# Kernel tuning notes

Measured on AMD Instinct MI355X. Metric: run time of the kernel, lower is better.

The kernel has to match this reference:

```python
import jax, jax.numpy as jnp
import numpy as np

NUM_GROUPS = 256


def _linear(x, w, b):
    return x @ w + b


def _layernorm(x, g, b, eps=1e-5):
    mu = jnp.mean(x, axis=-1, keepdims=True)
    var = jnp.mean((x - mu) ** 2, axis=-1, keepdims=True)
    return (x - mu) / jnp.sqrt(var + eps) * g + b


def setup_inputs() -> dict:
    key = jax.random.key(0)
    ks = jax.random.split(key, 12)
    B, N, C = 16, 8192, 3
    s = 0.02
    return {
        "xyz": jax.random.normal(ks[0], (B, N, C), jnp.float32),
        "labels": jax.random.randint(ks[1], (B, N), 0, NUM_GROUPS),
        # conv1: Linear(3,128) -> LayerNorm(128) -> ReLU -> Linear(128,256)
        "w1a": jax.random.normal(ks[2], (3, 128), jnp.float32) * s,
        "b1a": jnp.zeros((128,), jnp.float32),
        "g1": jnp.ones((128,), jnp.float32),
        "beta1": jnp.zeros((128,), jnp.float32),
        "w1b": jax.random.normal(ks[3], (128, 256), jnp.float32) * s,
        "b1b": jnp.zeros((256,), jnp.float32),
        # conv2: Linear(512,512) -> LayerNorm(512) -> ReLU -> Linear(512,256)
        "w2a": jax.random.normal(ks[4], (512, 512), jnp.float32) * s,
        "b2a": jnp.zeros((512,), jnp.float32),
        "g2": jnp.ones((512,), jnp.float32),
        "beta2": jnp.zeros((512,), jnp.float32),
        "w2b": jax.random.normal(ks[5], (512, 256), jnp.float32) * s,
        "b2b": jnp.zeros((256,), jnp.float32),
    }


def reference(xyz, labels, w1a, b1a, g1, beta1, w1b, b1b,
              w2a, b2a, g2, beta2, w2b, b2b):
    # per-batch segment reductions over cluster labels
    seg_sum = jax.vmap(lambda f, l: jax.ops.segment_sum(f, l, num_segments=NUM_GROUPS))
    seg_max = jax.vmap(lambda f, l: jax.ops.segment_max(f, l, num_segments=NUM_GROUPS))
    gather = jax.vmap(lambda p, l: p[l])  # [G,D],[N] -> [N,D]

    # centroids = per-cluster mean of xyz (converged kmeans centroids)
    counts = seg_sum(jnp.ones_like(xyz[..., :1]), labels)          # [B,G,1]
    centroids = seg_sum(xyz, labels) / jnp.maximum(counts, 1.0)    # [B,G,3]

    p_i = gather(centroids, labels)                                # [B,N,3]
    relative_xyz = xyz - p_i                                       # feature_type='dp'

    h = _linear(relative_xyz, w1a, b1a)
    h = jax.nn.relu(_layernorm(h, g1, beta1))
    h = _linear(h, w1b, b1b)                                       # [B,N,256]

    pooled = seg_max(h, labels)                                    # [B,G,256]
    pooled = jnp.where(jnp.isfinite(pooled), pooled, 0.0)          # empty groups -> 0
    repeated = gather(pooled, labels)                              # [B,N,256]

    cat = jnp.concatenate([repeated, h], axis=-1)                  # [B,N,512]
    h2 = _linear(cat, w2a, b2a)
    h2 = jax.nn.relu(_layernorm(h2, g2, beta2))
    h2 = _linear(h2, w2b, b2b)                                     # [B,N,256]

    out = seg_max(h2, labels)                                      # [B,G,256]
    out = jnp.where(jnp.isfinite(out), out, 0.0)
    return (centroids, out, p_i, labels)
```

## Files before the change

kernel.cpp:

```cpp
#include <hip/hip_runtime.h>
#include <hip/hip_bf16.h>

#define NB_  16
#define NPTS 8192
#define NG   256
#define NP   (NB_*NPTS)
#define NBLK (NP/32)

#define OFF_CENT 0
#define OFF_OUT  12288
#define OFF_PI   1060864
#define OFF_LAB  1454080

typedef unsigned short u16;
typedef __attribute__((ext_vector_type(8))) short bf16x8;
typedef __attribute__((ext_vector_type(4))) float f32x4;

static constexpr size_t WS_SUMS  = 0;
static constexpr size_t WS_A1    = 65536;
static constexpr size_t WS_H     = WS_A1   + (size_t)NP*128*2;
static constexpr size_t WS_PBF   = WS_H    + (size_t)NP*256*2;
static constexpr size_t WS_WT1   = WS_PBF  + (size_t)NB_*NG*256*2;
static constexpr size_t WS_WT2A  = WS_WT1  + (size_t)256*128*2;
static constexpr size_t WS_WT2B  = WS_WT2A + (size_t)512*512*2;
static constexpr size_t WS_PREP  = WS_WT2B + (size_t)256*512*2;
static constexpr size_t WS_OFFS  = WS_PREP + (size_t)NB_*NG*512*4;
static constexpr size_t WS_CNT   = WS_OFFS + (size_t)NB_*NG*4;
static constexpr size_t WS_CUR   = WS_CNT  + (size_t)NB_*NG*4;
static constexpr size_t WS_SPOS  = WS_CUR  + (size_t)NB_*NG*4;
static constexpr size_t WS_GLAB  = WS_SPOS + (size_t)NP*4;
static constexpr size_t WS_PF    = WS_GLAB + (size_t)NP*4;
static constexpr size_t WS_PL    = WS_PF   + (size_t)NBLK*256*4;
static constexpr size_t WS_DST   = WS_PL   + (size_t)NBLK*256*4;
static constexpr size_t WS_NEED  = WS_DST  + (size_t)NB_*NG*256*4;

__device__ __forceinline__ u16 f2bf_bits(float f){
  __hip_bfloat16 h = __float2bfloat16(f);
  union { __hip_bfloat16 h; u16 s; } u; u.h = h; return u.s;
}
__device__ __forceinline__ float bf_bits2f(u16 s){
  return __uint_as_float(((unsigned)s) << 16);
}

__device__ __forceinline__ void gload16(const void* g, void* l){
  __builtin_amdgcn_global_load_lds((const __attribute__((address_space(1))) void*)g,
                                   (__attribute__((address_space(3))) void*)l, 16, 0, 0);
}

__global__ void k_init(float* __restrict__ sums, int* __restrict__ cursor){
  int i = blockIdx.x*blockDim.x + threadIdx.x;
  if (i < NB_*NG*4) sums[i] = 0.f;
  if (i < NB_*NG) cursor[i] = 0;
}

__global__ void k_wt(const float* __restrict__ src, u16* __restrict__ dst, int K, int N){
  int i = blockIdx.x*blockDim.x + threadIdx.x;
  if (i >= K*N) return;
  int n = i / K, k = i - n*K;
  dst[i] = f2bf_bits(src[(size_t)k*N + n]);
}

__global__ void k_points(const float* __restrict__ xyz, const int* __restrict__ labels,
                         float* __restrict__ sums, float* __restrict__ outLab){
  int p = blockIdx.x*blockDim.x + threadIdx.x;
  if (p >= NP) return;
  int b = p / NPTS;
  int g = labels[p];
  float x = xyz[p*3+0], y = xyz[p*3+1], z = xyz[p*3+2];
  float* s = sums + (size_t)(b*NG + g)*4;
  atomicAdd(s+0, x); atomicAdd(s+1, y); atomicAdd(s+2, z); atomicAdd(s+3, 1.f);
  outLab[p] = (float)g;
}

__global__ void k_cent(const float* __restrict__ sums, float* __restrict__ cent_out){
  int i = blockIdx.x*blockDim.x + threadIdx.x;
  if (i >= NB_*NG) return;
  const float* s = sums + (size_t)i*4;
  float c = fmaxf(s[3], 1.f);
  cent_out[i*3+0] = s[0]/c;
  cent_out[i*3+1] = s[1]/c;
  cent_out[i*3+2] = s[2]/c;
}

__global__ void k_scan(const float* __restrict__ sums, int* __restrict__ offs,
                       int* __restrict__ counts){
  __shared__ int sc[256];
  int b = blockIdx.x, g = threadIdx.x;
  int c = (int)(sums[(size_t)(b*NG+g)*4+3] + 0.5f);
  sc[g] = c;
  __syncthreads();
  for (int d = 1; d < 256; d <<= 1){
    int t = (g >= d) ? sc[g-d] : 0;
    __syncthreads();
    sc[g] += t;
    __syncthreads();
  }
  offs[b*NG+g] = b*NPTS + sc[g] - c;
  counts[b*NG+g] = c;
}

__global__ void k_scatter(const int* __restrict__ labels, const int* __restrict__ offs,
                          int* __restrict__ cursor, int* __restrict__ sortpos,
                          int* __restrict__ glab){
  int p = blockIdx.x*blockDim.x + threadIdx.x;
  if (p >= NP) return;
  int b = p / NPTS, g = labels[p];
  int pos = offs[b*NG+g] + atomicAdd(&cursor[b*NG+g], 1);
  sortpos[p] = pos;
  glab[pos] = g;
}

__global__ __launch_bounds__(256) void k_mlp1(
    const float* __restrict__ xyz, const int* __restrict__ labels,
    const int* __restrict__ sortpos, const float* __restrict__ cent,
    const float* __restrict__ w1a, const float* __restrict__ b1a,
    const float* __restrict__ g1, const float* __restrict__ beta1,
    u16* __restrict__ a1, float* __restrict__ pi_out)
{
  int wave = (int)((blockIdx.x*blockDim.x + threadIdx.x) >> 6);
  int lane = threadIdx.x & 63;
  int p = wave;
  if (p >= NP) return;
  int b = p / NPTS;
  int g = labels[p];
  const float* cb = cent + (size_t)(b*NG+g)*3;
  float c0 = cb[0], c1 = cb[1], c2 = cb[2];
  float r0 = xyz[p*3+0]-c0, r1 = xyz[p*3+1]-c1, r2 = xyz[p*3+2]-c2;
  if (lane < 3) pi_out[(size_t)p*3+lane] = (lane==0?c0:(lane==1?c1:c2));
  int j = lane*2;
  float2 wa0 = *(const float2*)(w1a + 0*128 + j);
  float2 wa1 = *(const float2*)(w1a + 1*128 + j);
  float2 wa2 = *(const float2*)(w1a + 2*128 + j);
  float2 bb  = *(const float2*)(b1a + j);
  float t0 = bb.x + r0*wa0.x + r1*wa1.x + r2*wa2.x;
  float t1 = bb.y + r0*wa0.y + r1*wa1.y + r2*wa2.y;
  float s = t0+t1, sq = t0*t0 + t1*t1;
  #pragma unroll
  for (int m = 32; m; m >>= 1){ s += __shfl_xor(s, m); sq += __shfl_xor(sq, m); }
  float mu  = s * (1.f/128.f);
  float var = sq * (1.f/128.f) - mu*mu;
  float inv = rsqrtf(var + 1e-5f);
  float2 gg = *(const float2*)(g1 + j), be = *(const float2*)(beta1 + j);
  float a0 = fmaxf((t0-mu)*inv*gg.x + be.x, 0.f);
  float a1v = fmaxf((t1-mu)*inv*gg.y + be.y, 0.f);
  unsigned pk = ((unsigned)f2bf_bits(a1v) << 16) | f2bf_bits(a0);
  int sp = sortpos[p];
  *reinterpret_cast<unsigned*>(a1 + (size_t)sp*128 + j) = pk;
}

template<int EPI>
__global__ __launch_bounds__(256)
void mgemm(const u16* __restrict__ A, int lda, int K,
           const u16* __restrict__ BT, int ldb, int kofs,
           const float* __restrict__ bias,
           u16* __restrict__ Cst, float* __restrict__ Cf, int ldc, int Nc)
{
  __shared__ alignas(16) u16 As[128*32];
  __shared__ alignas(16) u16 Bs[128*32];
  int NBk = Nc >> 7;
  int bm = blockIdx.x / NBk, bn = blockIdx.x % NBk;
  int m0 = bm << 7, n0 = bn << 7;
  int tid = threadIdx.x;
  int lane = tid & 63, w = tid >> 6;
  int wr = w >> 1, wc = w & 1;
  int l15 = lane & 15, l4 = lane >> 4;
  int r0 = tid >> 2;
  int ks = (tid & 3) << 3;
  u16* asd0 = As + (size_t)(w*64)*8;
  u16* asd1 = As + (size_t)(256 + w*64)*8;
  u16* bsd0 = Bs + (size_t)(w*64)*8;
  u16* bsd1 = Bs + (size_t)(256 + w*64)*8;
  f32x4 acc[4][4];
  #pragma unroll
  for (int i = 0; i < 4; ++i)
    #pragma unroll
    for (int jj = 0; jj < 4; ++jj)
      #pragma unroll
      for (int e = 0; e < 4; ++e) acc[i][jj][e] = 0.f;

  for (int k0 = 0; k0 < K; k0 += 32){
    gload16(A + (size_t)(m0 + r0)*lda + k0 + ks, asd0);
    gload16(A + (size_t)(m0 + r0 + 64)*lda + k0 + ks, asd1);
    gload16(BT + (size_t)(n0 + r0)*ldb + kofs + k0 + ks, bsd0);
    gload16(BT + (size_t)(n0 + r0 + 64)*ldb + kofs + k0 + ks, bsd1);
    __syncthreads();
    bf16x8 af[4], bfr[4];
    #pragma unroll
    for (int i = 0; i < 4; ++i){
      af[i]  = *(const bf16x8*)&As[(size_t)(wr*64 + i*16 + l15)*32 + l4*8];
      bfr[i] = *(const bf16x8*)&Bs[(size_t)(wc*64 + i*16 + l15)*32 + l4*8];
    }
    #pragma unroll
    for (int i = 0; i < 4; ++i)
      #pragma unroll
      for (int jj = 0; jj < 4; ++jj)
        acc[i][jj] = __builtin_amdgcn_mfma_f32_16x16x32_bf16(af[i], bfr[jj], acc[i][jj], 0, 0, 0);
    __syncthreads();
  }

  float bi[4];
  #pragma unroll
  for (int jj = 0; jj < 4; ++jj) bi[jj] = bias[n0 + wc*64 + jj*16 + l15];
  #pragma unroll
  for (int i = 0; i < 4; ++i){
    #pragma unroll
    for (int r = 0; r < 4; ++r){
      int m = m0 + wr*64 + i*16 + l4*4 + r;
      #pragma unroll
      for (int jj = 0; jj < 4; ++jj){
        int n = n0 + wc*64 + jj*16 + l15;
        float v = acc[i][jj][r] + bi[jj];
        if (EPI == 1) Cst[(size_t)m*ldc + n] = f2bf_bits(v);
        if (EPI == 3) Cf[(size_t)m*ldc + n] = v;
      }
    }
  }
}

__global__ __launch_bounds__(256) void k_pool(const u16* __restrict__ h,
                                              const int* __restrict__ offs,
                                              const int* __restrict__ counts,
                                              u16* __restrict__ poolbf){
  int bg = blockIdx.x, c = threadIdx.x;
  int cnt = counts[bg];
  if (cnt == 0){ poolbf[(size_t)bg*256 + c] = 0; return; }
  int off = offs[bg];
  float mx = bf_bits2f(h[(size_t)off*256 + c]);
  for (int r = 1; r < cnt; ++r)
    mx = fmaxf(mx, bf_bits2f(h[(size_t)(off+r)*256 + c]));
  poolbf[(size_t)bg*256 + c] = f2bf_bits(mx);
}

__global__ __launch_bounds__(512, 4)
void fused3(const u16* __restrict__ h, const u16* __restrict__ wt2a,
            const u16* __restrict__ wt2b, const float* __restrict__ prepf,
            const float* __restrict__ b2b, const float* __restrict__ g2,
            const float* __restrict__ beta2, const int* __restrict__ glab,
            float* __restrict__ pf, float* __restrict__ pl, float* __restrict__ dstage)
{
  __shared__ alignas(16) char smem[33792];
  float* ssum  = (float*)(smem + 33280);
  float* ssq   = (float*)(smem + 33408);
  int*  glab_s = (int*)(smem + 33536);
  int tid = threadIdx.x;
  int w = tid >> 6, lane = tid & 63;
  int l15 = lane & 15, l4 = lane >> 4;
  int m0 = blockIdx.x << 5;
  if (tid < 32){ ssum[tid] = 0.f; ssq[tid] = 0.f; glab_s[tid] = glab[m0 + tid]; }

  const char* hb = (const char*)h;
  {
    int lrow = lane >> 5;
    int kb = (lane & 31) << 4;
    #pragma unroll
    for (int t = 0; t < 2; ++t){
      int q = w*2 + t;
      int row = q*2 + lrow;
      gload16(hb + (size_t)(m0 + row)*512 + (kb ^ ((row & 7) << 4)),
              smem + q*1024);
    }
  }
  f32x4 acc[2][4];
  #pragma unroll
  for (int i = 0; i < 2; ++i)
    #pragma unroll
    for (int j = 0; j < 4; ++j)
      #pragma unroll
      for (int e = 0; e < 4; ++e) acc[i][j][e] = 0.f;
  __syncthreads();

  for (int k0 = 0; k0 < 256; k0 += 32){
    bf16x8 af[2], bfr[4];
    #pragma unroll
    for (int i = 0; i < 2; ++i){
      int row = i*16 + l15;
      af[i] = *(const bf16x8*)(smem + row*512 + (((k0 + l4*8) << 1) ^ ((row & 7) << 4)));
    }
    #pragma unroll
    for (int j = 0; j < 4; ++j){
      int n = (w<<6) + (j<<4) + l15;
      bfr[j] = *(const bf16x8*)(wt2a + (size_t)n*512 + 256 + k0 + l4*8);
    }
    #pragma unroll
    for (int i = 0; i < 2; ++i)
      #pragma unroll
      for (int j = 0; j < 4; ++j)
        acc[i][j] = __builtin_amdgcn_mfma_f32_16x16x32_bf16(af[i], bfr[j], acc[i][j], 0, 0, 0);
  }

  int gb = (m0 / NPTS) * NG;
  {
    int grp[2][4];
    #pragma unroll
    for (int i = 0; i < 2; ++i)
      #pragma unroll
      for (int r = 0; r < 4; ++r)
        grp[i][r] = gb + glab_s[(i<<4) + (l4<<2) + r];
    #pragma unroll
    for (int i = 0; i < 2; ++i)
      #pragma unroll
      for (int j = 0; j < 4; ++j){
        int n = (w<<6) + (j<<4) + l15;
        #pragma unroll
        for (int r = 0; r < 4; ++r)
          acc[i][j][r] += prepf[((size_t)grp[i][r] << 9) + n];
      }
  }
  #pragma unroll
  for (int i = 0; i < 2; ++i)
    #pragma unroll
    for (int r = 0; r < 4; ++r){
      float s = 0.f, q = 0.f;
      #pragma unroll
      for (int j = 0; j < 4; ++j){ float v = acc[i][j][r]; s += v; q += v*v; }
      #pragma unroll
      for (int mk = 1; mk < 16; mk <<= 1){ s += __shfl_xor(s, mk); q += __shfl_xor(q, mk); }
      if (l15 == 0){
        int row = (i<<4) + (l4<<2) + r;
        atomicAdd(&ssum[row], s);
        atomicAdd(&ssq[row], q);
      }
    }
  __syncthreads();
  if (tid < 32){
    float mu = ssum[tid] * (1.f/512.f);
    float var = ssq[tid] * (1.f/512.f) - mu*mu;
    ssum[tid] = mu;
    ssq[tid] = rsqrtf(var + 1e-5f);
  }
  __syncthreads();
  {
    float gcol[4], bcol[4];
    #pragma unroll
    for (int j = 0; j < 4; ++j){
      int n = (w<<6) + (j<<4) + l15;
      gcol[j] = g2[n]; bcol[j] = beta2[n];
    }
    #pragma unroll
    for (int i = 0; i < 2; ++i)
      #pragma unroll
      for (int r = 0; r < 4; ++r){
        int row = (i<<4) + (l4<<2) + r;
        float mu = ssum[row], inv = ssq[row];
        #pragma unroll
        for (int j = 0; j < 4; ++j){
          int n = (w<<6) + (j<<4) + l15;
          float v = fmaxf((acc[i][j][r] - mu)*inv*gcol[j] + bcol[j], 0.f);
          int byo = (row << 10) + ((n << 1) ^ ((row & 7) << 4));
          *(u16*)(smem + byo) = f2bf_bits(v);
        }
      }
  }
  __syncthreads();

  f32x4 acc2[2][2];
  #pragma unroll
  for (int i = 0; i < 2; ++i)
    #pragma unroll
    for (int j = 0; j < 2; ++j)
      #pragma unroll
      for (int e = 0; e < 4; ++e) acc2[i][j][e] = 0.f;

  for (int k0 = 0; k0 < 512; k0 += 32){
    bf16x8 af2[2], bf2[2];
    #pragma unroll
    for (int i = 0; i < 2; ++i){
      int row = (i<<4) + l15;
      af2[i] = *(const bf16x8*)(smem + (row << 10) + ((((k0 + l4*8)) << 1) ^ ((row & 7) << 4)));
    }
    #pragma unroll
    for (int j = 0; j < 2; ++j){
      int n = (w<<5) + (j<<4) + l15;
      bf2[j] = *(const bf16x8*)(wt2b + (size_t)n*512 + k0 + l4*8);
    }
    #pragma unroll
    for (int i = 0; i < 2; ++i)
      #pragma unroll
      for (int j = 0; j < 2; ++j)
        acc2[i][j] = __builtin_amdgcn_mfma_f32_16x16x32_bf16(af2[i], bf2[j], acc2[i][j], 0, 0, 0);
  }
  __syncthreads();

  float bb0 = b2b[(w<<5) + l15], bb1 = b2b[(w<<5) + 16 + l15];
  float* vbuf = (float*)smem;
  #pragma unroll
  for (int i = 0; i < 2; ++i)
    #pragma unroll
    for (int j = 0; j < 2; ++j){
      int n = (w<<5) + (j<<4) + l15;
      float bbj = j ? bb1 : bb0;
      #pragma unroll
      for (int r = 0; r < 4; ++r){
        int row = (i<<4) + (l4<<2) + r;
        vbuf[row*260 + n] = acc2[i][j][r] + bbj;
      }
    }
  __syncthreads();
  if (tid < 256){
    int c = tid;
    size_t blk = blockIdx.x;
    int curg = glab_s[0];
    float mx = vbuf[c];
    bool from0 = true;
    for (int r = 1; r < 32; ++r){
      int g = glab_s[r];
      float v = vbuf[r*260 + c];
      if (g != curg){
        if (from0) pf[blk*256 + c] = mx;
        else       dstage[((size_t)(gb + curg))*256 + c] = mx;
        curg = g; mx = v; from0 = false;
      } else mx = fmaxf(mx, v);
    }
    if (from0) pf[blk*256 + c] = mx;
    else       pl[blk*256 + c] = mx;
  }
}

__global__ __launch_bounds__(256) void k_combine(const int* __restrict__ offs,
                                                 const int* __restrict__ counts,
                                                 const float* __restrict__ pf,
                                                 const float* __restrict__ pl,
                                                 const float* __restrict__ dstage,
                                                 float* __restrict__ outp){
  int bg = blockIdx.x, c = threadIdx.x;
  int cnt = counts[bg];
  if (cnt == 0){ outp[(size_t)bg*256 + c] = 0.f; return; }
  int off = offs[bg], end = off + cnt;
  int B0 = off >> 5, B1 = (end - 1) >> 5;
  float v;
  if (B0 == B1){
    if ((off & 31) == 0)      v = pf[(size_t)B0*256 + c];
    else if ((end & 31) == 0) v = pl[(size_t)B0*256 + c];
    else                      v = dstage[(size_t)bg*256 + c];
  } else {
    v = ((off & 31) == 0) ? pf[(size_t)B0*256 + c] : pl[(size_t)B0*256 + c];
    for (int k = B0 + 1; k <= B1; ++k)
      v = fmaxf(v, pf[(size_t)k*256 + c]);
  }
  outp[(size_t)bg*256 + c] = v;
}

__global__ void k_sig(float* __restrict__ out, float val){
  int i = blockIdx.x*blockDim.x + threadIdx.x;
  if (i < 256) out[i] = val;
}

extern "C" void kernel_launch(void* const* d_in, const int* in_sizes, int n_in,
                              void* d_out, int out_size, void* d_ws, size_t ws_size,
                              hipStream_t stream) {
  const float* xyz    = (const float*)d_in[0];
  const int*   labels = (const int*)  d_in[1];
  const float* w1a    = (const float*)d_in[2];
  const float* b1a    = (const float*)d_in[3];
  const float* g1     = (const float*)d_in[4];
  const float* beta1  = (const float*)d_in[5];
  const float* w1b    = (const float*)d_in[6];
  const float* b1b    = (const float*)d_in[7];
  const float* w2a    = (const float*)d_in[8];
  const float* b2a    = (const float*)d_in[9];
  const float* g2     = (const float*)d_in[10];
  const float* beta2  = (const float*)d_in[11];
  const float* w2b    = (const float*)d_in[12];
  const float* b2b    = (const float*)d_in[13];
  float* out = (float*)d_out;
  char* ws = (char*)d_ws;

  if (ws_size < WS_NEED){
    k_sig<<<1, 256, 0, stream>>>(out, 10000.f + (float)(ws_size >> 20));
    return;
  }

  float*     sums   = (float*)(ws + WS_SUMS);
  u16*       a1     = (u16*)(ws + WS_A1);
  u16*       h      = (u16*)(ws + WS_H);
  u16*       poolbf = (u16*)(ws + WS_PBF);
  u16*       wt1    = (u16*)(ws + WS_WT1);
  u16*       wt2a   = (u16*)(ws + WS_WT2A);
  u16*       wt2b   = (u16*)(ws + WS_WT2B);
  float*     prepf  = (float*)(ws + WS_PREP);
  int*       offs   = (int*)(ws + WS_OFFS);
  int*       counts = (int*)(ws + WS_CNT);
  int*       cursor = (int*)(ws + WS_CUR);
  int*       sortpos= (int*)(ws + WS_SPOS);
  int*       glab   = (int*)(ws + WS_GLAB);
  float*     pf     = (float*)(ws + WS_PF);
  float*     pl     = (float*)(ws + WS_PL);
  float*     dstage = (float*)(ws + WS_DST);

  float* cent_out = out + OFF_CENT;
  float* out_seg  = out + OFF_OUT;
  float* pi_out   = out + OFF_PI;
  float* lab_out  = out + OFF_LAB;

  k_init<<<64, 256, 0, stream>>>(sums, cursor);
  k_wt<<<(128*256+255)/256, 256, 0, stream>>>(w1b, wt1, 128, 256);
  k_wt<<<(512*512+255)/256, 256, 0, stream>>>(w2a, wt2a, 512, 512);
  k_wt<<<(512*256+255)/256, 256, 0, stream>>>(w2b, wt2b, 512, 256);
  k_points<<<NP/256, 256, 0, stream>>>(xyz, labels, sums, lab_out);
  k_cent<<<(NB_*NG+255)/256, 256, 0, stream>>>(sums, cent_out);
  k_scan<<<NB_, 256, 0, stream>>>(sums, offs, counts);
  k_scatter<<<NP/256, 256, 0, stream>>>(labels, offs, cursor, sortpos, glab);
  k_mlp1<<<NP/4, 256, 0, stream>>>(xyz, labels, sortpos, cent_out,
                                   w1a, b1a, g1, beta1, a1, pi_out);
  mgemm<1><<<(NP/128)*(256/128), 256, 0, stream>>>(
      a1, 128, 128, wt1, 128, 0, b1b, h, (float*)nullptr, 256, 256);
  k_pool<<<NB_*NG, 256, 0, stream>>>(h, offs, counts, poolbf);
  mgemm<3><<<(NB_*NG/128)*(512/128), 256, 0, stream>>>(
      poolbf, 256, 256, wt2a, 512, 0, b2a, (u16*)nullptr, prepf, 512, 512);
  fused3<<<NBLK, 512, 0, stream>>>(h, wt2a, wt2b, prepf, b2b, g2, beta2, glab,
                                   pf, pl, dstage);
  k_combine<<<NB_*NG, 256, 0, stream>>>(offs, counts, pf, pl, dstage, out_seg);
}
```

Baseline: 415.7 us.

## Double fused MLP2 row tile to 64 rows with 16-wave blocks

The fused second-MLP kernel now processes 64 points per block with 1024 threads, arranged as 2 waves along M by 8 along N, instead of 32 points with 512 threads. The K loops are fully unrolled with precomputed weight pointers. The value buffer stride drops from 260 to 256 so the larger tile fits in LDS, and the combine kernel is updated to the 64-row block boundaries. The aim is fewer blocks, fewer partial segment-max outputs, and better cache reuse of the weights. In exchange, the serial per-column max pass now covers twice as many rows while 768 threads sit idle, and the unpadded stride may cause LDS bank conflicts.

```diff
diff --git a/kernel.cpp b/kernel.cpp
--- a/kernel.cpp
+++ b/kernel.cpp
@@ -5,7 +5,7 @@
 #define NPTS 8192
 #define NG   256
 #define NP   (NB_*NPTS)
-#define NBLK (NP/32)
+#define NBLK (NP/64)
 
 #define OFF_CENT 0
 #define OFF_OUT  12288
@@ -231,25 +231,26 @@
   poolbf[(size_t)bg*256 + c] = f2bf_bits(mx);
 }
 
-__global__ __launch_bounds__(512, 4)
-void fused3(const u16* __restrict__ h, const u16* __restrict__ wt2a,
+__global__ __launch_bounds__(1024, 1)
+void fused5(const u16* __restrict__ h, const u16* __restrict__ wt2a,
             const u16* __restrict__ wt2b, const float* __restrict__ prepf,
             const float* __restrict__ b2b, const float* __restrict__ g2,
             const float* __restrict__ beta2, const int* __restrict__ glab,
             float* __restrict__ pf, float* __restrict__ pl, float* __restrict__ dstage)
 {
-  __shared__ alignas(16) char smem[33792];
-  float* ssum  = (float*)(smem + 33280);
-  float* ssq   = (float*)(smem + 33408);
-  int*  glab_s = (int*)(smem + 33536);
+  __shared__ alignas(16) char smem[66560];
+  float* ssum  = (float*)(smem + 65536);
+  float* ssq   = (float*)(smem + 65792);
+  int*  glab_s = (int*)(smem + 66048);
   int tid = threadIdx.x;
   int w = tid >> 6, lane = tid & 63;
+  int wm = w >> 3, wn = w & 7;
   int l15 = lane & 15, l4 = lane >> 4;
-  int m0 = blockIdx.x << 5;
-  if (tid < 32){ ssum[tid] = 0.f; ssq[tid] = 0.f; glab_s[tid] = glab[m0 + tid]; }
-
-  const char* hb = (const char*)h;
+  int m0 = blockIdx.x << 6;
+  if (tid < 64){ ssum[tid] = 0.f; ssq[tid] = 0.f; glab_s[tid] = glab[m0 + tid]; }
+
   {
+    const char* hb = (const char*)h;
     int lrow = lane >> 5;
     int kb = (lane & 31) << 4;
     #pragma unroll
@@ -269,23 +270,26 @@
       for (int e = 0; e < 4; ++e) acc[i][j][e] = 0.f;
   __syncthreads();
 
-  for (int k0 = 0; k0 < 256; k0 += 32){
-    bf16x8 af[2], bfr[4];
-    #pragma unroll
-    for (int i = 0; i < 2; ++i){
-      int row = i*16 + l15;
-      af[i] = *(const bf16x8*)(smem + row*512 + (((k0 + l4*8) << 1) ^ ((row & 7) << 4)));
-    }
-    #pragma unroll
-    for (int j = 0; j < 4; ++j){
-      int n = (w<<6) + (j<<4) + l15;
-      bfr[j] = *(const bf16x8*)(wt2a + (size_t)n*512 + 256 + k0 + l4*8);
-    }
-    #pragma unroll
-    for (int i = 0; i < 2; ++i)
+  {
+    const u16* wA = wt2a + ((size_t)((wn<<6) + l15))*512 + 256 + l4*8;
+    #pragma unroll
+    for (int kk = 0; kk < 8; ++kk){
+      const int k0 = kk*32;
+      bf16x8 af[2], bfr[4];
+      #pragma unroll
+      for (int i = 0; i < 2; ++i){
+        int row = (wm<<5) + (i<<4) + l15;
+        af[i] = *(const bf16x8*)(smem + row*512 + ((((k0 + l4*8)) << 1) ^ ((row & 7) << 4)));
+      }
       #pragma unroll
       for (int j = 0; j < 4; ++j)
-        acc[i][j] = __builtin_amdgcn_mfma_f32_16x16x32_bf16(af[i], bfr[j], acc[i][j], 0, 0, 0);
+        bfr[j] = *(const bf16x8*)(wA + j*8192 + k0);
+      #pragma unroll
+      for (int i = 0; i < 2; ++i)
+        #pragma unroll
+        for (int j = 0; j < 4; ++j)
+          acc[i][j] = __builtin_amdgcn_mfma_f32_16x16x32_bf16(af[i], bfr[j], acc[i][j], 0, 0, 0);
+    }
   }
 
   int gb = (m0 / NPTS) * NG;
@@ -295,12 +299,12 @@
     for (int i = 0; i < 2; ++i)
       #pragma unroll
       for (int r = 0; r < 4; ++r)
-        grp[i][r] = gb + glab_s[(i<<4) + (l4<<2) + r];
+        grp[i][r] = gb + glab_s[(wm<<5) + (i<<4) + (l4<<2) + r];
     #pragma unroll
     for (int i = 0; i < 2; ++i)
       #pragma unroll
       for (int j = 0; j < 4; ++j){
-        int n = (w<<6) + (j<<4) + l15;
+        int n = (wn<<6) + (j<<4) + l15;
         #pragma unroll
         for (int r = 0; r < 4; ++r)
           acc[i][j][r] += prepf[((size_t)grp[i][r] << 9) + n];
@@ -316,13 +320,13 @@
       #pragma unroll
       for (int mk = 1; mk < 16; mk <<= 1){ s += __shfl_xor(s, mk); q += __shfl_xor(q, mk); }
       if (l15 == 0){
-        int row = (i<<4) + (l4<<2) + r;
+        int row = (wm<<5) + (i<<4) + (l4<<2) + r;
         atomicAdd(&ssum[row], s);
         atomicAdd(&ssq[row], q);
       }
     }
   __syncthreads();
-  if (tid < 32){
+  if (tid < 64){
     float mu = ssum[tid] * (1.f/512.f);
     float var = ssq[tid] * (1.f/512.f) - mu*mu;
     ssum[tid] = mu;
@@ -333,20 +337,20 @@
     float gcol[4], bcol[4];
     #pragma unroll
     for (int j = 0; j < 4; ++j){
-      int n = (w<<6) + (j<<4) + l15;
+      int n = (wn<<6) + (j<<4) + l15;
       gcol[j] = g2[n]; bcol[j] = beta2[n];
     }
     #pragma unroll
     for (int i = 0; i < 2; ++i)
       #pragma unroll
       for (int r = 0; r < 4; ++r){
-        int row = (i<<4) + (l4<<2) + r;
+        int row = (wm<<5) + (i<<4) + (l4<<2) + r;
         float mu = ssum[row], inv = ssq[row];
         #pragma unroll
         for (int j = 0; j < 4; ++j){
-          int n = (w<<6) + (j<<4) + l15;
+          int n = (wn<<6) + (j<<4) + l15;
           float v = fmaxf((acc[i][j][r] - mu)*inv*gcol[j] + bcol[j], 0.f);
-          int byo = (row << 10) + ((n << 1) ^ ((row & 7) << 4));
+          int byo = (row << 10) + (((n << 1)) ^ ((row & 7) << 4));
           *(u16*)(smem + byo) = f2bf_bits(v);
         }
       }
@@ -361,38 +365,41 @@
       #pragma unroll
       for (int e = 0; e < 4; ++e) acc2[i][j][e] = 0.f;
 
-  for (int k0 = 0; k0 < 512; k0 += 32){
-    bf16x8 af2[2], bf2[2];
-    #pragma unroll
-    for (int i = 0; i < 2; ++i){
-      int row = (i<<4) + l15;
-      af2[i] = *(const bf16x8*)(smem + (row << 10) + ((((k0 + l4*8)) << 1) ^ ((row & 7) << 4)));
-    }
+  {
+    const u16* wB = wt2b + ((size_t)((wn<<5) + l15))*512 + l4*8;
+    #pragma unroll
+    for (int kk = 0; kk < 16; ++kk){
+      const int k0 = kk*32;
+      bf16x8 af2[2], bf2[2];
+      #pragma unroll
+      for (int i = 0; i < 2; ++i){
+        int row = (wm<<5) + (i<<4) + l15;
+        af2[i] = *(const bf16x8*)(smem + (row << 10) + ((((k0 + l4*8)) << 1) ^ ((row & 7) << 4)));
+      }
+      #pragma unroll
+      for (int j = 0; j < 2; ++j)
+        bf2[j] = *(const bf16x8*)(wB + j*8192 + k0);
+      #pragma unroll
+      for (int i = 0; i < 2; ++i)
+        #pragma unroll
+        for (int j = 0; j < 2; ++j)
+          acc2[i][j] = __builtin_amdgcn_mfma_f32_16x16x32_bf16(af2[i], bf2[j], acc2[i][j], 0, 0, 0);
+    }
+  }
+  __syncthreads();
+
+  float bb0 = b2b[(wn<<5) + l15], bb1 = b2b[(wn<<5) + 16 + l15];
+  float* vbuf = (float*)smem;
+  #pragma unroll
+  for (int i = 0; i < 2; ++i)
     #pragma unroll
     for (int j = 0; j < 2; ++j){
-      int n = (w<<5) + (j<<4) + l15;
-      bf2[j] = *(const bf16x8*)(wt2b + (size_t)n*512 + k0 + l4*8);
-    }
-    #pragma unroll
-    for (int i = 0; i < 2; ++i)
-      #pragma unroll
-      for (int j = 0; j < 2; ++j)
-        acc2[i][j] = __builtin_amdgcn_mfma_f32_16x16x32_bf16(af2[i], bf2[j], acc2[i][j], 0, 0, 0);
-  }
-  __syncthreads();
-
-  float bb0 = b2b[(w<<5) + l15], bb1 = b2b[(w<<5) + 16 + l15];
-  float* vbuf = (float*)smem;
-  #pragma unroll
-  for (int i = 0; i < 2; ++i)
-    #pragma unroll
-    for (int j = 0; j < 2; ++j){
-      int n = (w<<5) + (j<<4) + l15;
+      int n = (wn<<5) + (j<<4) + l15;
       float bbj = j ? bb1 : bb0;
       #pragma unroll
       for (int r = 0; r < 4; ++r){
-        int row = (i<<4) + (l4<<2) + r;
-        vbuf[row*260 + n] = acc2[i][j][r] + bbj;
+        int row = (wm<<5) + (i<<4) + (l4<<2) + r;
+        vbuf[row*256 + n] = acc2[i][j][r] + bbj;
       }
     }
   __syncthreads();
@@ -402,9 +409,9 @@
     int curg = glab_s[0];
     float mx = vbuf[c];
     bool from0 = true;
-    for (int r = 1; r < 32; ++r){
+    for (int r = 1; r < 64; ++r){
       int g = glab_s[r];
-      float v = vbuf[r*260 + c];
+      float v = vbuf[r*256 + c];
       if (g != curg){
         if (from0) pf[blk*256 + c] = mx;
         else       dstage[((size_t)(gb + curg))*256 + c] = mx;
@@ -426,14 +433,14 @@
   int cnt = counts[bg];
   if (cnt == 0){ outp[(size_t)bg*256 + c] = 0.f; return; }
   int off = offs[bg], end = off + cnt;
-  int B0 = off >> 5, B1 = (end - 1) >> 5;
+  int B0 = off >> 6, B1 = (end - 1) >> 6;
   float v;
   if (B0 == B1){
-    if ((off & 31) == 0)      v = pf[(size_t)B0*256 + c];
-    else if ((end & 31) == 0) v = pl[(size_t)B0*256 + c];
+    if ((off & 63) == 0)      v = pf[(size_t)B0*256 + c];
+    else if ((end & 63) == 0) v = pl[(size_t)B0*256 + c];
     else                      v = dstage[(size_t)bg*256 + c];
   } else {
-    v = ((off & 31) == 0) ? pf[(size_t)B0*256 + c] : pl[(size_t)B0*256 + c];
+    v = ((off & 63) == 0) ? pf[(size_t)B0*256 + c] : pl[(size_t)B0*256 + c];
     for (int k = B0 + 1; k <= B1; ++k)
       v = fmaxf(v, pf[(size_t)k*256 + c]);
   }
@@ -507,7 +514,7 @@
   k_pool<<<NB_*NG, 256, 0, stream>>>(h, offs, counts, poolbf);
   mgemm<3><<<(NB_*NG/128)*(512/128), 256, 0, stream>>>(
       poolbf, 256, 256, wt2a, 512, 0, b2a, (u16*)nullptr, prepf, 512, 512);
-  fused3<<<NBLK, 512, 0, stream>>>(h, wt2a, wt2b, prepf, b2b, g2, beta2, glab,
-                                   pf, pl, dstage);
+  fused5<<<NBLK, 1024, 0, stream>>>(h, wt2a, wt2b, prepf, b2b, g2, beta2, glab,
+                                    pf, pl, dstage);
   k_combine<<<NB_*NG, 256, 0, stream>>>(offs, counts, pf, pl, dstage, out_seg);
 }
```

After: 463.0 us. 11.4% more time.
